# Performance work log

Hardware: AMD Instinct MI355X
Metric: run time of the kernel (lower is better)

Reference implementation:

```python
import jax, jax.numpy as jnp
import numpy as np

B, N = 64, 4096

def setup_inputs() -> dict:
    key = jax.random.key(0)
    k1, k2, k3, k4, k5, k6 = jax.random.split(key, 6)
    return {
        "V_mag": jax.random.uniform(k1, (B, N), dtype=jnp.float32, minval=0.9, maxval=1.1),
        "V_ang": 0.3 * jax.random.normal(k2, (B, N), dtype=jnp.float32),
        "P_in": jax.random.normal(k3, (B, N), dtype=jnp.float32),
        "Q_in": jax.random.normal(k4, (B, N), dtype=jnp.float32),
        "G_bus": jax.random.normal(k5, (N, N), dtype=jnp.float32) / np.sqrt(N),
        "B_bus": jax.random.normal(k6, (N, N), dtype=jnp.float32) / np.sqrt(N),
    }

def reference(V_mag, V_ang, P_in, Q_in, G_bus, B_bus):
    # P_i = V_i sum_j V_j (G_ij cos(ti-tj) + B_ij sin(ti-tj))
    # Q_i = V_i sum_j V_j (G_ij sin(ti-tj) - B_ij cos(ti-tj))
    # Angle-addition rewrite (exact): with c_j = V_j cos(t_j), s_j = V_j sin(t_j):
    #   sum_j G_ij V_j cos(ti-tj) = cos(ti)*(G c)_i + sin(ti)*(G s)_i, etc.
    cos_t = jnp.cos(V_ang)  # [B, N]
    sin_t = jnp.sin(V_ang)
    c = V_mag * cos_t       # V_j cos(t_j)
    s = V_mag * sin_t       # V_j sin(t_j)
    Gc = jnp.einsum('ij,bj->bi', G_bus, c)
    Gs = jnp.einsum('ij,bj->bi', G_bus, s)
    Bc = jnp.einsum('ij,bj->bi', B_bus, c)
    Bs = jnp.einsum('ij,bj->bi', B_bus, s)
    # sum_j V_j (G cos + B sin) = cos_ti*(Gc+Bs) + sin_ti*(Gs-Bc)
    P_calc = V_mag * (cos_t * (Gc + Bs) + sin_t * (Gs - Bc))
    # sum_j V_j (G sin - B cos) = sin_ti*(Gc+Bs) - cos_ti*(Gs-Bc)
    Q_calc = V_mag * (sin_t * (Gc + Bs) - cos_t * (Gs - Bc))
    res_P = P_calc - P_in
    res_Q = Q_calc - Q_in
    return (res_P, res_Q)
```

## Files before the change

kernel.cpp:

```cpp
#include <hip/hip_runtime.h>
#include <stdint.h>

#define N_DIM 4096
#define B_DIM 64

typedef __bf16 bf16x8 __attribute__((ext_vector_type(8)));
typedef float floatx4 __attribute__((ext_vector_type(4)));

union FragU { uint4 u; bf16x8 h; };

__device__ __forceinline__ unsigned short f2bf_rne(float f) {
    unsigned int u = __float_as_uint(f);
    u += 0x7fffu + ((u >> 16) & 1u);
    return (unsigned short)(u >> 16);
}

__global__ __launch_bounds__(256) void pf_prep(
        const float* __restrict__ Vmag, const float* __restrict__ Vang,
        unsigned short* __restrict__ c_pk, unsigned short* __restrict__ s_pk) {
    int idx = blockIdx.x * 256 + threadIdx.x;
    int b = idx >> 12;
    int j = idx & 4095;
    float sv, cv;
    sincosf(Vang[idx], &sv, &cv);
    float v = Vmag[idx];
    int p = (((j >> 3) << 6) + b) * 8 + (j & 7);
    c_pk[p] = f2bf_rne(v * cv);
    s_pk[p] = f2bf_rne(v * sv);
}

__global__ __launch_bounds__(1024) void pf_gemm(
        const float* __restrict__ G, const float* __restrict__ Bm,
        const unsigned short* __restrict__ c_pk, const unsigned short* __restrict__ s_pk,
        const float* __restrict__ Vmag, const float* __restrict__ Vang,
        const float* __restrict__ P_in, const float* __restrict__ Q_in,
        float* __restrict__ out) {
    __shared__ __align__(16) float red[2 * 8 * 16 * 66];
    const int tid = threadIdx.x;
    const int wave = tid >> 6;
    const int lane = tid & 63;
    const int n = lane & 15;
    const int quad = lane >> 4;
    const int i0 = blockIdx.x << 4;

    const float* gp = G  + (size_t)(i0 + n) * N_DIM + wave * 256 + quad * 8;
    const float* bp = Bm + (size_t)(i0 + n) * N_DIM + wave * 256 + quad * 8;
    const unsigned short* cp = c_pk + ((size_t)(wave * 32 + quad) * 64 + n) * 8;
    const unsigned short* sp = s_pk + ((size_t)(wave * 32 + quad) * 64 + n) * 8;

    floatx4 accX[4], accY[4];
    #pragma unroll
    for (int t = 0; t < 4; ++t) {
        accX[t] = (floatx4){0.f, 0.f, 0.f, 0.f};
        accY[t] = (floatx4){0.f, 0.f, 0.f, 0.f};
    }

    float4 g0 = *(const float4*)(gp);
    float4 g1 = *(const float4*)(gp + 4);
    float4 h0 = *(const float4*)(bp);
    float4 h1 = *(const float4*)(bp + 4);

    #pragma unroll
    for (int t = 0; t < 8; ++t) {
        float4 ng0, ng1, nh0, nh1;
        if (t < 7) {
            const float* g2 = gp + (t + 1) * 32;
            const float* b2 = bp + (t + 1) * 32;
            ng0 = *(const float4*)(g2);
            ng1 = *(const float4*)(g2 + 4);
            nh0 = *(const float4*)(b2);
            nh1 = *(const float4*)(b2 + 4);
        }

        bf16x8 ag, ah;
        ag[0] = (__bf16)g0.x; ag[1] = (__bf16)g0.y; ag[2] = (__bf16)g0.z; ag[3] = (__bf16)g0.w;
        ag[4] = (__bf16)g1.x; ag[5] = (__bf16)g1.y; ag[6] = (__bf16)g1.z; ag[7] = (__bf16)g1.w;
        ah[0] = (__bf16)h0.x; ah[1] = (__bf16)h0.y; ah[2] = (__bf16)h0.z; ah[3] = (__bf16)h0.w;
        ah[4] = (__bf16)h1.x; ah[5] = (__bf16)h1.y; ah[6] = (__bf16)h1.z; ah[7] = (__bf16)h1.w;

        const unsigned short* cpt = cp + (size_t)t * 2048;
        const unsigned short* spt = sp + (size_t)t * 2048;

        uint4 cu[4];
        #pragma unroll
        for (int t16 = 0; t16 < 4; ++t16) cu[t16] = *(const uint4*)(cpt + t16 * 128);
        #pragma unroll
        for (int t16 = 0; t16 < 4; ++t16) {
            FragU cf, nf;
            cf.u = cu[t16];
            nf.u.x = cu[t16].x ^ 0x80008000u;
            nf.u.y = cu[t16].y ^ 0x80008000u;
            nf.u.z = cu[t16].z ^ 0x80008000u;
            nf.u.w = cu[t16].w ^ 0x80008000u;
            accX[t16] = __builtin_amdgcn_mfma_f32_16x16x32_bf16(ag, cf.h, accX[t16], 0, 0, 0);
            accY[t16] = __builtin_amdgcn_mfma_f32_16x16x32_bf16(ah, nf.h, accY[t16], 0, 0, 0);
        }

        uint4 su[4];
        #pragma unroll
        for (int t16 = 0; t16 < 4; ++t16) su[t16] = *(const uint4*)(spt + t16 * 128);
        #pragma unroll
        for (int t16 = 0; t16 < 4; ++t16) {
            FragU sf;
            sf.u = su[t16];
            accX[t16] = __builtin_amdgcn_mfma_f32_16x16x32_bf16(ah, sf.h, accX[t16], 0, 0, 0);
            accY[t16] = __builtin_amdgcn_mfma_f32_16x16x32_bf16(ag, sf.h, accY[t16], 0, 0, 0);
        }

        g0 = ng0; g1 = ng1; h0 = nh0; h1 = nh1;
    }

    #define RED(x, wp, m, b) red[(((x) * 8 + (wp)) * 16 + (m)) * 66 + (b)]
    if (wave >= 8) {
        #pragma unroll
        for (int t = 0; t < 4; ++t)
            #pragma unroll
            for (int r = 0; r < 4; ++r) {
                RED(0, wave - 8, (quad << 2) + r, (t << 4) + n) = accX[t][r];
                RED(1, wave - 8, (quad << 2) + r, (t << 4) + n) = accY[t][r];
            }
    }
    __syncthreads();
    if (wave < 8) {
        #pragma unroll
        for (int t = 0; t < 4; ++t)
            #pragma unroll
            for (int r = 0; r < 4; ++r) {
                RED(0, wave, (quad << 2) + r, (t << 4) + n) += accX[t][r];
                RED(1, wave, (quad << 2) + r, (t << 4) + n) += accY[t][r];
            }
    }
    __syncthreads();

    {
        int bb = tid >> 4;
        int m = tid & 15;
        float X = 0.f, Y = 0.f;
        #pragma unroll
        for (int w = 0; w < 8; ++w) {
            X += RED(0, w, m, bb);
            Y += RED(1, w, m, bb);
        }
        size_t off = (size_t)bb * N_DIM + i0 + m;
        float sv, cv;
        sincosf(Vang[off], &sv, &cv);
        float v = Vmag[off];
        float c = v * cv;
        float s = v * sv;
        out[off] = c * X + s * Y - P_in[off];
        out[(size_t)B_DIM * N_DIM + off] = s * X - c * Y - Q_in[off];
    }
}

extern "C" void kernel_launch(void* const* d_in, const int* in_sizes, int n_in,
                              void* d_out, int out_size, void* d_ws, size_t ws_size,
                              hipStream_t stream) {
    const float* Vmag = (const float*)d_in[0];
    const float* Vang = (const float*)d_in[1];
    const float* P_in = (const float*)d_in[2];
    const float* Q_in = (const float*)d_in[3];
    const float* G    = (const float*)d_in[4];
    const float* Bm   = (const float*)d_in[5];
    float* out = (float*)d_out;

    char* ws = (char*)d_ws;
    unsigned short* c_pk = (unsigned short*)(ws);
    unsigned short* s_pk = (unsigned short*)(ws + (512u << 10));

    hipLaunchKernelGGL(pf_prep, dim3((B_DIM * N_DIM) / 256), dim3(256), 0, stream,
                       Vmag, Vang, c_pk, s_pk);
    hipLaunchKernelGGL(pf_gemm, dim3(N_DIM / 16), dim3(1024), 0, stream,
                       G, Bm, c_pk, s_pk, Vmag, Vang, P_in, Q_in, out);
}
```

Measured before the change: 174.3 us.

## Split batch columns across wave pairs and prefetch c/s fragments

```diff
diff --git a/kernel.cpp b/kernel.cpp
--- a/kernel.cpp
+++ b/kernel.cpp
@@ -35,57 +35,64 @@
         const float* __restrict__ Vmag, const float* __restrict__ Vang,
         const float* __restrict__ P_in, const float* __restrict__ Q_in,
         float* __restrict__ out) {
-    __shared__ __align__(16) float red[2 * 8 * 16 * 66];
+    __shared__ __align__(16) float red[2 * 4 * 16 * 66];
     const int tid = threadIdx.x;
     const int wave = tid >> 6;
     const int lane = tid & 63;
     const int n = lane & 15;
     const int quad = lane >> 4;
+    const int ch = wave & 1;
+    const int w8 = wave >> 1;
     const int i0 = blockIdx.x << 4;
 
-    const float* gp = G  + (size_t)(i0 + n) * N_DIM + wave * 256 + quad * 8;
-    const float* bp = Bm + (size_t)(i0 + n) * N_DIM + wave * 256 + quad * 8;
-    const unsigned short* cp = c_pk + ((size_t)(wave * 32 + quad) * 64 + n) * 8;
-    const unsigned short* sp = s_pk + ((size_t)(wave * 32 + quad) * 64 + n) * 8;
+    const float* gp = G  + (size_t)(i0 + n) * N_DIM + w8 * 512 + quad * 8;
+    const float* bp = Bm + (size_t)(i0 + n) * N_DIM + w8 * 512 + quad * 8;
+    const unsigned short* cp = c_pk + ((size_t)((w8 * 64 + quad) * 64) + ch * 32 + n) * 8;
+    const unsigned short* sp = s_pk + ((size_t)((w8 * 64 + quad) * 64) + ch * 32 + n) * 8;
 
-    floatx4 accX[4], accY[4];
+    floatx4 accX[2], accY[2];
     #pragma unroll
-    for (int t = 0; t < 4; ++t) {
-        accX[t] = (floatx4){0.f, 0.f, 0.f, 0.f};
-        accY[t] = (floatx4){0.f, 0.f, 0.f, 0.f};
+    for (int t16 = 0; t16 < 2; ++t16) {
+        accX[t16] = (floatx4){0.f, 0.f, 0.f, 0.f};
+        accY[t16] = (floatx4){0.f, 0.f, 0.f, 0.f};
     }
 
     float4 g0 = *(const float4*)(gp);
     float4 g1 = *(const float4*)(gp + 4);
     float4 h0 = *(const float4*)(bp);
     float4 h1 = *(const float4*)(bp + 4);
+    uint4 cu[2], su[2];
+    cu[0] = *(const uint4*)(cp);
+    cu[1] = *(const uint4*)(cp + 128);
+    su[0] = *(const uint4*)(sp);
+    su[1] = *(const uint4*)(sp + 128);
 
     #pragma unroll
-    for (int t = 0; t < 8; ++t) {
-        float4 ng0, ng1, nh0, nh1;
-        if (t < 7) {
-            const float* g2 = gp + (t + 1) * 32;
-            const float* b2 = bp + (t + 1) * 32;
-            ng0 = *(const float4*)(g2);
-            ng1 = *(const float4*)(g2 + 4);
-            nh0 = *(const float4*)(b2);
-            nh1 = *(const float4*)(b2 + 4);
-        }
-
+    for (int t = 0; t < 16; ++t) {
         bf16x8 ag, ah;
         ag[0] = (__bf16)g0.x; ag[1] = (__bf16)g0.y; ag[2] = (__bf16)g0.z; ag[3] = (__bf16)g0.w;
         ag[4] = (__bf16)g1.x; ag[5] = (__bf16)g1.y; ag[6] = (__bf16)g1.z; ag[7] = (__bf16)g1.w;
         ah[0] = (__bf16)h0.x; ah[1] = (__bf16)h0.y; ah[2] = (__bf16)h0.z; ah[3] = (__bf16)h0.w;
         ah[4] = (__bf16)h1.x; ah[5] = (__bf16)h1.y; ah[6] = (__bf16)h1.z; ah[7] = (__bf16)h1.w;
 
-        const unsigned short* cpt = cp + (size_t)t * 2048;
-        const unsigned short* spt = sp + (size_t)t * 2048;
+        uint4 ncu[2], nsu[2];
+        if (t < 15) {
+            const float* g2 = gp + (t + 1) * 32;
+            const float* b2 = bp + (t + 1) * 32;
+            g0 = *(const float4*)(g2);
+            g1 = *(const float4*)(g2 + 4);
+            h0 = *(const float4*)(b2);
+            h1 = *(const float4*)(b2 + 4);
+            const unsigned short* cpt = cp + (size_t)(t + 1) * 2048;
+            const unsigned short* spt = sp + (size_t)(t + 1) * 2048;
+            ncu[0] = *(const uint4*)(cpt);
+            ncu[1] = *(const uint4*)(cpt + 128);
+            nsu[0] = *(const uint4*)(spt);
+            nsu[1] = *(const uint4*)(spt + 128);
+        }
 
-        uint4 cu[4];
         #pragma unroll
-        for (int t16 = 0; t16 < 4; ++t16) cu[t16] = *(const uint4*)(cpt + t16 * 128);
-        #pragma unroll
-        for (int t16 = 0; t16 < 4; ++t16) {
+        for (int t16 = 0; t16 < 2; ++t16) {
             FragU cf, nf;
             cf.u = cu[t16];
             nf.u.x = cu[t16].x ^ 0x80008000u;
@@ -95,39 +102,38 @@
             accX[t16] = __builtin_amdgcn_mfma_f32_16x16x32_bf16(ag, cf.h, accX[t16], 0, 0, 0);
             accY[t16] = __builtin_amdgcn_mfma_f32_16x16x32_bf16(ah, nf.h, accY[t16], 0, 0, 0);
         }
-
-        uint4 su[4];
         #pragma unroll
-        for (int t16 = 0; t16 < 4; ++t16) su[t16] = *(const uint4*)(spt + t16 * 128);
-        #pragma unroll
-        for (int t16 = 0; t16 < 4; ++t16) {
+        for (int t16 = 0; t16 < 2; ++t16) {
             FragU sf;
             sf.u = su[t16];
             accX[t16] = __builtin_amdgcn_mfma_f32_16x16x32_bf16(ah, sf.h, accX[t16], 0, 0, 0);
             accY[t16] = __builtin_amdgcn_mfma_f32_16x16x32_bf16(ag, sf.h, accY[t16], 0, 0, 0);
         }
 
-        g0 = ng0; g1 = ng1; h0 = nh0; h1 = nh1;
+        if (t < 15) {
+            cu[0] = ncu[0]; cu[1] = ncu[1];
+            su[0] = nsu[0]; su[1] = nsu[1];
+        }
     }
 
-    #define RED(x, wp, m, b) red[(((x) * 8 + (wp)) * 16 + (m)) * 66 + (b)]
-    if (wave >= 8) {
+    #define RED(x, wp, m, b) red[(((x) * 4 + (wp)) * 16 + (m)) * 66 + (b)]
+    if (w8 >= 4) {
         #pragma unroll
-        for (int t = 0; t < 4; ++t)
+        for (int t16 = 0; t16 < 2; ++t16)
             #pragma unroll
             for (int r = 0; r < 4; ++r) {
-                RED(0, wave - 8, (quad << 2) + r, (t << 4) + n) = accX[t][r];
-                RED(1, wave - 8, (quad << 2) + r, (t << 4) + n) = accY[t][r];
+                RED(0, w8 - 4, (quad << 2) + r, ch * 32 + (t16 << 4) + n) = accX[t16][r];
+                RED(1, w8 - 4, (quad << 2) + r, ch * 32 + (t16 << 4) + n) = accY[t16][r];
             }
     }
     __syncthreads();
-    if (wave < 8) {
+    if (w8 < 4) {
         #pragma unroll
-        for (int t = 0; t < 4; ++t)
+        for (int t16 = 0; t16 < 2; ++t16)
             #pragma unroll
             for (int r = 0; r < 4; ++r) {
-                RED(0, wave, (quad << 2) + r, (t << 4) + n) += accX[t][r];
-                RED(1, wave, (quad << 2) + r, (t << 4) + n) += accY[t][r];
+                RED(0, w8, (quad << 2) + r, ch * 32 + (t16 << 4) + n) += accX[t16][r];
+                RED(1, w8, (quad << 2) + r, ch * 32 + (t16 << 4) + n) += accY[t16][r];
             }
     }
     __syncthreads();
@@ -137,7 +143,7 @@
         int m = tid & 15;
         float X = 0.f, Y = 0.f;
         #pragma unroll
-        for (int w = 0; w < 8; ++w) {
+        for (int w = 0; w < 4; ++w) {
             X += RED(0, w, m, bb);
             Y += RED(1, w, m, bb);
         }
```

Result: no change. 175.8 us (+0.9%).

## Restructure GEMM into 64-row split-K tiles with LDS double-buffering and atomic reduction

Applied to the files above, without the earlier changes.

```diff
diff --git a/kernel.cpp b/kernel.cpp
--- a/kernel.cpp
+++ b/kernel.cpp
@@ -3,11 +3,19 @@
 
 #define N_DIM 4096
 #define B_DIM 64
+#define BN (B_DIM * N_DIM)
 
 typedef __bf16 bf16x8 __attribute__((ext_vector_type(8)));
 typedef float floatx4 __attribute__((ext_vector_type(4)));
 
 union FragU { uint4 u; bf16x8 h; };
+
+#define AS1 __attribute__((address_space(1)))
+#define AS3 __attribute__((address_space(3)))
+
+__device__ __forceinline__ void gll16(const void* gp, void* lp) {
+    __builtin_amdgcn_global_load_lds((const AS1 void*)gp, (AS3 void*)lp, 16, 0, 0);
+}
 
 __device__ __forceinline__ unsigned short f2bf_rne(float f) {
     unsigned int u = __float_as_uint(f);
@@ -17,7 +25,8 @@
 
 __global__ __launch_bounds__(256) void pf_prep(
         const float* __restrict__ Vmag, const float* __restrict__ Vang,
-        unsigned short* __restrict__ c_pk, unsigned short* __restrict__ s_pk) {
+        unsigned short* __restrict__ c_pk, unsigned short* __restrict__ s_pk,
+        float* __restrict__ XY) {
     int idx = blockIdx.x * 256 + threadIdx.x;
     int b = idx >> 12;
     int j = idx & 4095;
@@ -27,129 +36,120 @@
     int p = (((j >> 3) << 6) + b) * 8 + (j & 7);
     c_pk[p] = f2bf_rne(v * cv);
     s_pk[p] = f2bf_rne(v * sv);
+    XY[idx] = 0.f;
+    XY[idx + BN] = 0.f;
 }
 
+#define BUFB 49152
+#define ABOFF 16384
+#define COFF 32768
+#define SOFF 40960
 __global__ __launch_bounds__(1024) void pf_gemm(
         const float* __restrict__ G, const float* __restrict__ Bm,
         const unsigned short* __restrict__ c_pk, const unsigned short* __restrict__ s_pk,
-        const float* __restrict__ Vmag, const float* __restrict__ Vang,
-        const float* __restrict__ P_in, const float* __restrict__ Q_in,
-        float* __restrict__ out) {
-    __shared__ __align__(16) float red[2 * 8 * 16 * 66];
+        float* __restrict__ XY) {
+    __shared__ __align__(16) char lds[2 * BUFB];
     const int tid = threadIdx.x;
     const int wave = tid >> 6;
     const int lane = tid & 63;
     const int n = lane & 15;
     const int quad = lane >> 4;
-    const int i0 = blockIdx.x << 4;
+    const int mt = wave >> 2;
+    const int nt = wave & 3;
+    const int rb = blockIdx.x & 63;
+    const int kq = blockIdx.x >> 6;
+    const int i0 = rb << 6;
+    const int k0 = kq << 10;
 
-    const float* gp = G  + (size_t)(i0 + n) * N_DIM + wave * 256 + quad * 8;
-    const float* bp = Bm + (size_t)(i0 + n) * N_DIM + wave * 256 + quad * 8;
-    const unsigned short* cp = c_pk + ((size_t)(wave * 32 + quad) * 64 + n) * 8;
-    const unsigned short* sp = s_pk + ((size_t)(wave * 32 + quad) * 64 + n) * 8;
+    const int rg = (wave << 2) + (lane >> 4);
+    const int gslot = (lane & 15) ^ (rg & 7);
+    const float* gsrc = G  + (size_t)(i0 + rg) * N_DIM + k0 + gslot * 4;
+    const float* bsrc = Bm + (size_t)(i0 + rg) * N_DIM + k0 + gslot * 4;
+    const unsigned short* csbase = (wave < 8) ? c_pk : s_pk;
+    const unsigned short* cssrc = csbase + ((size_t)(kq * 128 + (wave & 7)) << 9) + lane * 8;
+    char* stgA = lds + wave * 1024;
+    char* stgC = lds + COFF + ((wave >= 8) ? (SOFF - COFF) : 0) + (wave & 7) * 1024;
 
-    floatx4 accX[4], accY[4];
-    #pragma unroll
-    for (int t = 0; t < 4; ++t) {
-        accX[t] = (floatx4){0.f, 0.f, 0.f, 0.f};
-        accY[t] = (floatx4){0.f, 0.f, 0.f, 0.f};
+    const int r = (mt << 4) + n;
+    const int r7 = n & 7;
+    const int arow = r << 8;
+    const int csl = ((nt << 4) + n) << 4;
+
+    floatx4 accX = (floatx4){0.f, 0.f, 0.f, 0.f};
+    floatx4 accY = (floatx4){0.f, 0.f, 0.f, 0.f};
+
+    gll16(gsrc, stgA);
+    gll16(bsrc, stgA + ABOFF);
+    gll16(cssrc, stgC);
+
+    for (int ch = 0; ch < 16; ++ch) {
+        const int buf = (ch & 1) * BUFB;
+        __syncthreads();
+
+        if (ch < 15) {
+            const int nb = ((ch + 1) & 1) * BUFB;
+            gll16(gsrc + (ch + 1) * 64, stgA + nb);
+            gll16(bsrc + (ch + 1) * 64, stgA + nb + ABOFF);
+            gll16(cssrc + (size_t)(ch + 1) * 4096, stgC + nb);
+        }
+
+        const char* base = lds + buf;
+        #pragma unroll
+        for (int kk = 0; kk < 2; ++kk) {
+            const int u = (kk << 3) + (quad << 1);
+            const int s0 = u ^ r7;
+            const int s1 = s0 ^ 1;
+            float4 g0 = *(const float4*)(base + arow + s0 * 16);
+            float4 g1 = *(const float4*)(base + arow + s1 * 16);
+            float4 h0 = *(const float4*)(base + ABOFF + arow + s0 * 16);
+            float4 h1 = *(const float4*)(base + ABOFF + arow + s1 * 16);
+            bf16x8 ag, ah;
+            ag[0] = (__bf16)g0.x; ag[1] = (__bf16)g0.y; ag[2] = (__bf16)g0.z; ag[3] = (__bf16)g0.w;
+            ag[4] = (__bf16)g1.x; ag[5] = (__bf16)g1.y; ag[6] = (__bf16)g1.z; ag[7] = (__bf16)g1.w;
+            ah[0] = (__bf16)h0.x; ah[1] = (__bf16)h0.y; ah[2] = (__bf16)h0.z; ah[3] = (__bf16)h0.w;
+            ah[4] = (__bf16)h1.x; ah[5] = (__bf16)h1.y; ah[6] = (__bf16)h1.z; ah[7] = (__bf16)h1.w;
+
+            const int kgo = ((kk << 2) + quad) << 10;
+            FragU cf, sf, nf;
+            cf.u = *(const uint4*)(base + COFF + kgo + csl);
+            sf.u = *(const uint4*)(base + SOFF + kgo + csl);
+            nf.u.x = cf.u.x ^ 0x80008000u;
+            nf.u.y = cf.u.y ^ 0x80008000u;
+            nf.u.z = cf.u.z ^ 0x80008000u;
+            nf.u.w = cf.u.w ^ 0x80008000u;
+
+            accX = __builtin_amdgcn_mfma_f32_16x16x32_bf16(ag, cf.h, accX, 0, 0, 0);
+            accY = __builtin_amdgcn_mfma_f32_16x16x32_bf16(ah, nf.h, accY, 0, 0, 0);
+            accX = __builtin_amdgcn_mfma_f32_16x16x32_bf16(ah, sf.h, accX, 0, 0, 0);
+            accY = __builtin_amdgcn_mfma_f32_16x16x32_bf16(ag, sf.h, accY, 0, 0, 0);
+        }
     }
 
-    float4 g0 = *(const float4*)(gp);
-    float4 g1 = *(const float4*)(gp + 4);
-    float4 h0 = *(const float4*)(bp);
-    float4 h1 = *(const float4*)(bp + 4);
+    float* Xg = XY;
+    float* Yg = XY + BN;
+    const int ib = i0 + (mt << 4) + (quad << 2);
+    const int bb = (nt << 4) + n;
+    #pragma unroll
+    for (int rr = 0; rr < 4; ++rr) {
+        atomicAdd(Xg + (size_t)bb * N_DIM + ib + rr, accX[rr]);
+        atomicAdd(Yg + (size_t)bb * N_DIM + ib + rr, accY[rr]);
+    }
+}
 
-    #pragma unroll
-    for (int t = 0; t < 8; ++t) {
-        float4 ng0, ng1, nh0, nh1;
-        if (t < 7) {
-            const float* g2 = gp + (t + 1) * 32;
-            const float* b2 = bp + (t + 1) * 32;
-            ng0 = *(const float4*)(g2);
-            ng1 = *(const float4*)(g2 + 4);
-            nh0 = *(const float4*)(b2);
-            nh1 = *(const float4*)(b2 + 4);
-        }
-
-        bf16x8 ag, ah;
-        ag[0] = (__bf16)g0.x; ag[1] = (__bf16)g0.y; ag[2] = (__bf16)g0.z; ag[3] = (__bf16)g0.w;
-        ag[4] = (__bf16)g1.x; ag[5] = (__bf16)g1.y; ag[6] = (__bf16)g1.z; ag[7] = (__bf16)g1.w;
-        ah[0] = (__bf16)h0.x; ah[1] = (__bf16)h0.y; ah[2] = (__bf16)h0.z; ah[3] = (__bf16)h0.w;
-        ah[4] = (__bf16)h1.x; ah[5] = (__bf16)h1.y; ah[6] = (__bf16)h1.z; ah[7] = (__bf16)h1.w;
-
-        const unsigned short* cpt = cp + (size_t)t * 2048;
-        const unsigned short* spt = sp + (size_t)t * 2048;
-
-        uint4 cu[4];
-        #pragma unroll
-        for (int t16 = 0; t16 < 4; ++t16) cu[t16] = *(const uint4*)(cpt + t16 * 128);
-        #pragma unroll
-        for (int t16 = 0; t16 < 4; ++t16) {
-            FragU cf, nf;
-            cf.u = cu[t16];
-            nf.u.x = cu[t16].x ^ 0x80008000u;
-            nf.u.y = cu[t16].y ^ 0x80008000u;
-            nf.u.z = cu[t16].z ^ 0x80008000u;
-            nf.u.w = cu[t16].w ^ 0x80008000u;
-            accX[t16] = __builtin_amdgcn_mfma_f32_16x16x32_bf16(ag, cf.h, accX[t16], 0, 0, 0);
-            accY[t16] = __builtin_amdgcn_mfma_f32_16x16x32_bf16(ah, nf.h, accY[t16], 0, 0, 0);
-        }
-
-        uint4 su[4];
-        #pragma unroll
-        for (int t16 = 0; t16 < 4; ++t16) su[t16] = *(const uint4*)(spt + t16 * 128);
-        #pragma unroll
-        for (int t16 = 0; t16 < 4; ++t16) {
-            FragU sf;
-            sf.u = su[t16];
-            accX[t16] = __builtin_amdgcn_mfma_f32_16x16x32_bf16(ah, sf.h, accX[t16], 0, 0, 0);
-            accY[t16] = __builtin_amdgcn_mfma_f32_16x16x32_bf16(ag, sf.h, accY[t16], 0, 0, 0);
-        }
-
-        g0 = ng0; g1 = ng1; h0 = nh0; h1 = nh1;
-    }
-
-    #define RED(x, wp, m, b) red[(((x) * 8 + (wp)) * 16 + (m)) * 66 + (b)]
-    if (wave >= 8) {
-        #pragma unroll
-        for (int t = 0; t < 4; ++t)
-            #pragma unroll
-            for (int r = 0; r < 4; ++r) {
-                RED(0, wave - 8, (quad << 2) + r, (t << 4) + n) = accX[t][r];
-                RED(1, wave - 8, (quad << 2) + r, (t << 4) + n) = accY[t][r];
-            }
-    }
-    __syncthreads();
-    if (wave < 8) {
-        #pragma unroll
-        for (int t = 0; t < 4; ++t)
-            #pragma unroll
-            for (int r = 0; r < 4; ++r) {
-                RED(0, wave, (quad << 2) + r, (t << 4) + n) += accX[t][r];
-                RED(1, wave, (quad << 2) + r, (t << 4) + n) += accY[t][r];
-            }
-    }
-    __syncthreads();
-
-    {
-        int bb = tid >> 4;
-        int m = tid & 15;
-        float X = 0.f, Y = 0.f;
-        #pragma unroll
-        for (int w = 0; w < 8; ++w) {
-            X += RED(0, w, m, bb);
-            Y += RED(1, w, m, bb);
-        }
-        size_t off = (size_t)bb * N_DIM + i0 + m;
-        float sv, cv;
-        sincosf(Vang[off], &sv, &cv);
-        float v = Vmag[off];
-        float c = v * cv;
-        float s = v * sv;
-        out[off] = c * X + s * Y - P_in[off];
-        out[(size_t)B_DIM * N_DIM + off] = s * X - c * Y - Q_in[off];
-    }
+__global__ __launch_bounds__(256) void pf_epi(
+        const float* __restrict__ Vmag, const float* __restrict__ Vang,
+        const float* __restrict__ P_in, const float* __restrict__ Q_in,
+        const float* __restrict__ XY, float* __restrict__ out) {
+    int idx = blockIdx.x * 256 + threadIdx.x;
+    float X = XY[idx];
+    float Y = XY[idx + BN];
+    float sv, cv;
+    sincosf(Vang[idx], &sv, &cv);
+    float v = Vmag[idx];
+    float c = v * cv;
+    float s = v * sv;
+    out[idx] = c * X + s * Y - P_in[idx];
+    out[idx + BN] = s * X - c * Y - Q_in[idx];
 }
 
 extern "C" void kernel_launch(void* const* d_in, const int* in_sizes, int n_in,
@@ -166,9 +166,12 @@
     char* ws = (char*)d_ws;
     unsigned short* c_pk = (unsigned short*)(ws);
     unsigned short* s_pk = (unsigned short*)(ws + (512u << 10));
+    float* XY = (float*)(ws + (1u << 20));
 
-    hipLaunchKernelGGL(pf_prep, dim3((B_DIM * N_DIM) / 256), dim3(256), 0, stream,
-                       Vmag, Vang, c_pk, s_pk);
-    hipLaunchKernelGGL(pf_gemm, dim3(N_DIM / 16), dim3(1024), 0, stream,
-                       G, Bm, c_pk, s_pk, Vmag, Vang, P_in, Q_in, out);
+    hipLaunchKernelGGL(pf_prep, dim3(BN / 256), dim3(256), 0, stream,
+                       Vmag, Vang, c_pk, s_pk, XY);
+    hipLaunchKernelGGL(pf_gemm, dim3(256), dim3(1024), 0, stream,
+                       G, Bm, c_pk, s_pk, XY);
+    hipLaunchKernelGGL(pf_epi, dim3(BN / 256), dim3(256), 0, stream,
+                       Vmag, Vang, P_in, Q_in, XY, out);
 }
```

Result: slower. 195.5 us (+12.2%).
